# Kernel optimization log

Measured on AMD Instinct MI355X. Metric: run time of the kernel, lower is better.

## Reference

```python
import jax, jax.numpy as jnp
import numpy as np

AH, AW = 7, 7            # aligned_height, aligned_width
SCALE = 0.0625           # spatial_scale = 1/16


def setup_inputs() -> dict:
    key = jax.random.key(0)
    k1, k2, k3, k4, k5 = jax.random.split(key, 5)
    B, C, H, W = 2, 256, 64, 64
    N = 8000
    features = jax.random.normal(k1, (B, C, H, W), dtype=jnp.float32)
    img_h, img_w = H / SCALE, W / SCALE
    cx = jax.random.uniform(k2, (N,), minval=0.0, maxval=img_w)
    cy = jax.random.uniform(k3, (N,), minval=0.0, maxval=img_h)
    wh = jax.random.uniform(k4, (N, 2), minval=32.0, maxval=256.0)
    x1 = jnp.clip(cx - wh[:, 0] * 0.5, 0.0, img_w - 1.0)
    x2 = jnp.clip(cx + wh[:, 0] * 0.5, 0.0, img_w - 1.0)
    y1 = jnp.clip(cy - wh[:, 1] * 0.5, 0.0, img_h - 1.0)
    y2 = jnp.clip(cy + wh[:, 1] * 0.5, 0.0, img_h - 1.0)
    bidx = jax.random.randint(k5, (N,), 0, B).astype(jnp.float32)
    rois = jnp.stack([bidx, x1, y1, x2, y2], axis=1)  # [N,5]
    return {"features": features, "rois": rois}


def reference(features, rois):
    # features: [B,C,H,W]; rois: [N,5] = (batch_idx, x1, y1, x2, y2)
    B, C, H, W = features.shape
    b = rois[:, 0].astype(jnp.int32)                      # [N]
    x1 = rois[:, 1] * SCALE
    y1 = rois[:, 2] * SCALE
    x2 = rois[:, 3] * SCALE
    y2 = rois[:, 4] * SCALE
    bin_h = jnp.maximum(y2 - y1, 0.0) / (AH - 1)          # [N]
    bin_w = jnp.maximum(x2 - x1, 0.0) / (AW - 1)
    ph = jnp.arange(AH, dtype=jnp.float32)
    pw = jnp.arange(AW, dtype=jnp.float32)
    h = y1[:, None, None] + ph[None, :, None] * bin_h[:, None, None]  # [N,AH,1]
    w = x1[:, None, None] + pw[None, None, :] * bin_w[:, None, None]  # [N,1,AW]
    valid = (h >= 0) & (h < H) & (w >= 0) & (w < W)       # [N,AH,AW]
    h0 = jnp.clip(jnp.floor(h), 0, H - 2).astype(jnp.int32)
    w0 = jnp.clip(jnp.floor(w), 0, W - 2).astype(jnp.int32)
    lh = h - h0.astype(jnp.float32)                        # [N,AH,1]
    lw = w - w0.astype(jnp.float32)                        # [N,1,AW]
    f = jnp.transpose(features, (0, 2, 3, 1))              # [B,H,W,C]
    bi = b[:, None, None]                                  # [N,1,1]
    v00 = f[bi, h0, w0]                                    # [N,AH,AW,C]
    v01 = f[bi, h0, w0 + 1]
    v10 = f[bi, h0 + 1, w0]
    v11 = f[bi, h0 + 1, w0 + 1]
    out = (v00 * ((1 - lh) * (1 - lw))[..., None]
           + v10 * (lh * (1 - lw))[..., None]
           + v01 * ((1 - lh) * lw)[..., None]
           + v11 * (lh * lw)[..., None])                   # [N,AH,AW,C]
    out = jnp.where(valid[..., None], out, 0.0)
    return jnp.transpose(out, (0, 3, 1, 2))                # [N,C,AH,AW]
```

## Files before the change

kernel.cpp:

```cpp
#include <hip/hip_runtime.h>

#define AHH 7
#define AWW 7
#define NS 49
#define CC 256
#define HH 64
#define WW 64
#define CCH 64
#define NCHUNK (CC / CCH)
#define ELEMS_PER_ROI (CC * NS)
#define ELEMS_PER_CHUNK (CCH * NS)
#define VEC4_PER_CHUNK (ELEMS_PER_CHUNK / 4)
#define RSTRIDE 53
#define FT_ELEMS (2 * HH * WW * CC)
#define TS 64

typedef float v4f __attribute__((ext_vector_type(4)));

__global__ __launch_bounds__(256) void transpose_tiled(
    const float* __restrict__ A, float* __restrict__ AT) {
  const int bid = blockIdx.x;
  const int st  = bid & 63;
  const int ct  = (bid >> 6) & 3;
  const int b   = bid >> 8;
  const int tid = threadIdx.x;
  const int col = tid & 63;
  const int r0  = tid >> 6;

  __shared__ float tile[TS][TS + 1];

  const float* Ab  = A  + (size_t)b * CC * HH * WW;
  float*       ATb = AT + (size_t)b * HH * WW * CC;

#pragma unroll
  for (int k = 0; k < 16; ++k) {
    int r = r0 + (k << 2);
    tile[r][col] = Ab[(size_t)(ct * TS + r) * (HH * WW) + st * TS + col];
  }
  __syncthreads();
#pragma unroll
  for (int k = 0; k < 16; ++k) {
    int r = r0 + (k << 2);
    ATb[(size_t)(st * TS + r) * CC + ct * TS + col] = tile[col][r];
  }
}

__global__ __launch_bounds__(256) void roialign_t_kernel(
    const float* __restrict__ fT,
    const float* __restrict__ rois,
    float* __restrict__ out) {
  const int bid   = blockIdx.x;
  const int n     = bid >> 2;
  const int chunk = bid & 3;
  const int c0    = chunk * CCH;
  const int tid   = threadIdx.x;

  __shared__ float s_w[4][NS];
  __shared__ int   s_poff[NS];
  __shared__ int   s_base;
  __shared__ float s_res[CCH * RSTRIDE];

  if (tid < NS) {
    const float* roi = rois + n * 5;
    float bf = roi[0];
    float x1 = roi[1] * 0.0625f;
    float y1 = roi[2] * 0.0625f;
    float x2 = roi[3] * 0.0625f;
    float y2 = roi[4] * 0.0625f;
    float bin_h = fmaxf(y2 - y1, 0.0f) * (1.0f / 6.0f);
    float bin_w = fmaxf(x2 - x1, 0.0f) * (1.0f / 6.0f);
    int ph = tid / AWW;
    int pw = tid - ph * AWW;
    float h = y1 + (float)ph * bin_h;
    float w = x1 + (float)pw * bin_w;
    bool valid = (h >= 0.0f) && (h < (float)HH) && (w >= 0.0f) && (w < (float)WW);
    int h0 = min(max((int)floorf(h), 0), HH - 2);
    int w0 = min(max((int)floorf(w), 0), WW - 2);
    float lh = h - (float)h0;
    float lw = w - (float)w0;
    float w00 = (1.0f - lh) * (1.0f - lw);
    float w01 = (1.0f - lh) * lw;
    float w10 = lh * (1.0f - lw);
    float w11 = lh * lw;
    if (!valid) { w00 = 0.0f; w01 = 0.0f; w10 = 0.0f; w11 = 0.0f; }
    s_poff[tid] = (h0 * WW + w0) * CC;
    s_w[0][tid] = w00; s_w[1][tid] = w01; s_w[2][tid] = w10; s_w[3][tid] = w11;
    if (tid == 0) s_base = (int)bf * (HH * WW * CC);
  }
  __syncthreads();

  const float* fb = fT + s_base + c0;

#pragma unroll
  for (int it = 0; it < 4; ++it) {
    int wk = it * 256 + tid;
    int s  = wk >> 4;
    if (s < NS) {
      int q  = wk & 15;
      const float* p = fb + s_poff[s] + (q << 2);
      v4f v00 = *(const v4f*)(p);
      v4f v01 = *(const v4f*)(p + CC);
      v4f v10 = *(const v4f*)(p + WW * CC);
      v4f v11 = *(const v4f*)(p + WW * CC + CC);
      v4f r = v00 * s_w[0][s] + v01 * s_w[1][s] + v10 * s_w[2][s] + v11 * s_w[3][s];
      int base = (q << 2) * RSTRIDE + s;
      s_res[base]               = r.x;
      s_res[base + RSTRIDE]     = r.y;
      s_res[base + 2 * RSTRIDE] = r.z;
      s_res[base + 3 * RSTRIDE] = r.w;
      if (s < 3) {
        int dbase = base - RSTRIDE + 49;
        if (q > 0) s_res[dbase] = r.x;
        s_res[dbase + RSTRIDE]     = r.y;
        s_res[dbase + 2 * RSTRIDE] = r.z;
        s_res[dbase + 3 * RSTRIDE] = r.w;
      }
    }
  }
  __syncthreads();

  v4f* ob = (v4f*)(out + (size_t)n * ELEMS_PER_ROI + (size_t)c0 * NS);
#pragma unroll
  for (int it = 0; it < 4; ++it) {
    int i = it * 256 + tid;
    if (i < VEC4_PER_CHUNK) {
      int f0 = i * 4;
      int cl = f0 / NS;
      const v4f val = *(const v4f*)(s_res + f0 + 4 * cl);
      __builtin_nontemporal_store(val, &ob[i]);
    }
  }
}

__global__ __launch_bounds__(256) void roialign_fallback_kernel(
    const float* __restrict__ features,
    const float* __restrict__ rois,
    float* __restrict__ out) {
  const int n   = blockIdx.x;
  const int tid = threadIdx.x;
  __shared__ int   s_off[NS];
  __shared__ float s_w00[NS], s_w01[NS], s_w10[NS], s_w11[NS];
  __shared__ int   s_base;
  if (tid < NS) {
    const float* roi = rois + n * 5;
    float bf = roi[0];
    float x1 = roi[1] * 0.0625f, y1 = roi[2] * 0.0625f;
    float x2 = roi[3] * 0.0625f, y2 = roi[4] * 0.0625f;
    float bin_h = fmaxf(y2 - y1, 0.0f) * (1.0f / 6.0f);
    float bin_w = fmaxf(x2 - x1, 0.0f) * (1.0f / 6.0f);
    int ph = tid / AWW, pw = tid - ph * AWW;
    float h = y1 + (float)ph * bin_h, w = x1 + (float)pw * bin_w;
    bool valid = (h >= 0.0f) && (h < (float)HH) && (w >= 0.0f) && (w < (float)WW);
    int h0 = min(max((int)floorf(h), 0), HH - 2);
    int w0 = min(max((int)floorf(w), 0), WW - 2);
    float lh = h - (float)h0, lw = w - (float)w0;
    float w00 = (1.0f - lh) * (1.0f - lw), w01 = (1.0f - lh) * lw;
    float w10 = lh * (1.0f - lw), w11 = lh * lw;
    if (!valid) { w00 = w01 = w10 = w11 = 0.0f; }
    s_off[tid] = h0 * WW + w0;
    s_w00[tid] = w00; s_w01[tid] = w01; s_w10[tid] = w10; s_w11[tid] = w11;
    if (tid == 0) s_base = (int)bf * (CC * HH * WW);
  }
  __syncthreads();
  const float* fb = features + s_base;
  v4f* ob = (v4f*)(out + (size_t)n * ELEMS_PER_ROI);
  for (int i = tid; i < ELEMS_PER_ROI / 4; i += 256) {
    int f0 = i * 4;
    float r[4];
#pragma unroll
    for (int j = 0; j < 4; ++j) {
      int f = f0 + j;
      int c = f / NS;
      int s = f - c * NS;
      int off = s_off[s];
      const float* p = fb + (c << 12) + off;
      r[j] = p[0] * s_w00[s] + p[1] * s_w01[s] + p[WW] * s_w10[s] + p[WW + 1] * s_w11[s];
    }
    v4f val = {r[0], r[1], r[2], r[3]};
    __builtin_nontemporal_store(val, &ob[i]);
  }
}

extern "C" void kernel_launch(void* const* d_in, const int* in_sizes, int n_in,
                              void* d_out, int out_size, void* d_ws, size_t ws_size,
                              hipStream_t stream) {
  const float* features = (const float*)d_in[0];
  const float* rois     = (const float*)d_in[1];
  float* out            = (float*)d_out;
  int N = in_sizes[1] / 5;

  if (ws_size >= (size_t)FT_ELEMS * sizeof(float)) {
    float* fT = (float*)d_ws;
    transpose_tiled<<<2 * 4 * 64, 256, 0, stream>>>(features, fT);
    roialign_t_kernel<<<N * NCHUNK, 256, 0, stream>>>(fT, rois, out);
  } else {
    roialign_fallback_kernel<<<N, 256, 0, stream>>>(features, rois, out);
  }
}
```

Measured before the change: 86.22 us.

## Interleave ROIs by batch index so consecutive blocks hit alternating feature maps

Adds an extra block to the transpose kernel that computes a permutation of ROIs, alternating even and odd positions between batch 0 and batch 1 ROIs via a prefix-sum scan. The ROI-align kernel then processes ROIs in this permuted order. The intent appears to be balancing memory traffic across the two transposed feature maps, which could improve cache or channel locality. It adds a serial single-block scan and an indirect load per block. The scan handles at most 8192 ROIs (256 threads times 32), and larger N would leave part of the permutation unwritten.

```diff
diff --git a/kernel.cpp b/kernel.cpp
--- a/kernel.cpp
+++ b/kernel.cpp
@@ -17,15 +17,68 @@
 
 typedef float v4f __attribute__((ext_vector_type(4)));
 
-__global__ __launch_bounds__(256) void transpose_tiled(
-    const float* __restrict__ A, float* __restrict__ AT) {
+__global__ __launch_bounds__(256) void transpose_and_perm(
+    const float* __restrict__ A, float* __restrict__ AT,
+    const float* __restrict__ rois, int* __restrict__ perm, int N) {
+  const int tid = threadIdx.x;
+
+  if (blockIdx.x == 512) {
+    __shared__ int s_cnt[256];
+    __shared__ int s_n0;
+    const int EVENS = (N + 1) >> 1;
+    const int ODDS  = N >> 1;
+    const int i0 = tid * 32;
+    unsigned int flags = 0;
+    int c0 = 0;
+#pragma unroll
+    for (int k = 0; k < 32; ++k) {
+      int i = i0 + k;
+      int b = 1;
+      if (i < N) {
+        b = (int)rois[i * 5];
+        if (b == 0) c0++;
+      }
+      flags |= (unsigned)(b & 1) << k;
+    }
+    s_cnt[tid] = c0;
+    __syncthreads();
+    for (int d = 1; d < 256; d <<= 1) {
+      int v = (tid >= d) ? s_cnt[tid - d] : 0;
+      __syncthreads();
+      s_cnt[tid] += v;
+      __syncthreads();
+    }
+    int incl = s_cnt[tid];
+    int off0 = incl - c0;
+    if (tid == 255) s_n0 = incl;
+    __syncthreads();
+    const int n0 = s_n0;
+    const int n1 = N - n0;
+    int r0 = off0;
+    int r1 = min(i0, N) - off0;
+    for (int k = 0; k < 32; ++k) {
+      int i = i0 + k;
+      if (i >= N) break;
+      int b = (flags >> k) & 1;
+      int g;
+      if (b == 0) {
+        int r = r0++;
+        g = (r < EVENS) ? (2 * r) : (2 * (n1 + r - EVENS) + 1);
+      } else {
+        int r = r1++;
+        g = (r < ODDS) ? (2 * r + 1) : (2 * (n0 + r - ODDS));
+      }
+      perm[g] = i;
+    }
+    return;
+  }
+
   const int bid = blockIdx.x;
   const int st  = bid & 63;
   const int ct  = (bid >> 6) & 3;
   const int b   = bid >> 8;
-  const int tid = threadIdx.x;
   const int col = tid & 63;
-  const int r0  = tid >> 6;
+  const int r0_ = tid >> 6;
 
   __shared__ float tile[TS][TS + 1];
 
@@ -34,13 +87,13 @@
 
 #pragma unroll
   for (int k = 0; k < 16; ++k) {
-    int r = r0 + (k << 2);
+    int r = r0_ + (k << 2);
     tile[r][col] = Ab[(size_t)(ct * TS + r) * (HH * WW) + st * TS + col];
   }
   __syncthreads();
 #pragma unroll
   for (int k = 0; k < 16; ++k) {
-    int r = r0 + (k << 2);
+    int r = r0_ + (k << 2);
     ATb[(size_t)(st * TS + r) * CC + ct * TS + col] = tile[col][r];
   }
 }
@@ -48,9 +101,10 @@
 __global__ __launch_bounds__(256) void roialign_t_kernel(
     const float* __restrict__ fT,
     const float* __restrict__ rois,
+    const int* __restrict__ perm,
     float* __restrict__ out) {
   const int bid   = blockIdx.x;
-  const int n     = bid >> 2;
+  const int n     = perm[bid >> 2];
   const int chunk = bid & 3;
   const int c0    = chunk * CCH;
   const int tid   = threadIdx.x;
@@ -189,10 +243,12 @@
   float* out            = (float*)d_out;
   int N = in_sizes[1] / 5;
 
-  if (ws_size >= (size_t)FT_ELEMS * sizeof(float)) {
-    float* fT = (float*)d_ws;
-    transpose_tiled<<<2 * 4 * 64, 256, 0, stream>>>(features, fT);
-    roialign_t_kernel<<<N * NCHUNK, 256, 0, stream>>>(fT, rois, out);
+  size_t need = (size_t)FT_ELEMS * sizeof(float) + (size_t)N * sizeof(int);
+  if (ws_size >= need) {
+    float* fT  = (float*)d_ws;
+    int*  perm = (int*)((float*)d_ws + FT_ELEMS);
+    transpose_and_perm<<<513, 256, 0, stream>>>(features, fT, rois, perm, N);
+    roialign_t_kernel<<<N * NCHUNK, 256, 0, stream>>>(fT, rois, perm, out);
   } else {
     roialign_fallback_kernel<<<N, 256, 0, stream>>>(features, rois, out);
   }
```

New measurement: 90.21 us. +4.6%, slower.
